# Kernel tuning notes

Hardware: AMD Instinct MI355X
Metric: run time of the kernel (lower is better)

The kernel has to match this reference:

```python
import jax, jax.numpy as jnp
import numpy as np

TRIANGLE_TABLE = np.array([
    [-1,-1,-1,-1,-1,-1],[1,0,2,-1,-1,-1],[4,0,3,-1,-1,-1],[1,4,2,1,3,4],
    [3,1,5,-1,-1,-1],[2,3,0,2,5,3],[1,4,0,1,5,4],[4,2,5,-1,-1,-1],
    [4,5,2,-1,-1,-1],[4,1,0,4,5,1],[3,2,0,3,5,2],[1,3,5,-1,-1,-1],
    [4,1,2,4,3,1],[3,0,4,-1,-1,-1],[2,0,1,-1,-1,-1],[-1,-1,-1,-1,-1,-1]], dtype=np.int32)
NUM_TRI_TABLE = np.array([0,1,1,2,1,2,2,1,1,2,2,1,2,1,1,0], dtype=np.int32)
BASE_TET_EDGES = np.array([0,1,0,2,0,3,1,2,1,3,2,3], dtype=np.int32)

NV = 200_000
NT = 800_000

def setup_inputs() -> dict:
    key = jax.random.key(0)
    k1, k2, k3 = jax.random.split(key, 3)
    pos_nx3 = jax.random.normal(k1, (NV, 3), dtype=jnp.float32)
    sdf_n = jax.random.normal(k2, (NV,), dtype=jnp.float32)
    tet_fx4 = jax.random.randint(k3, (NT, 4), 0, NV, dtype=jnp.int32)
    return {"pos_nx3": pos_nx3, "sdf_n": sdf_n, "tet_fx4": tet_fx4}

def map_uv(face_gidx, max_idx):
    # Faithful port of DMTet.map_uv: one 2-triangle UV quad per (potential) tet.
    N = int(np.ceil(np.sqrt((max_idx + 1) // 2)))
    lin = jnp.linspace(0.0, 1.0 - 1.0 / N, N, dtype=jnp.float32)
    tex_y, tex_x = jnp.meshgrid(lin, lin, indexing='ij')
    pad = 0.9 / N
    uvs = jnp.stack([tex_x, tex_y, tex_x + pad, tex_y,
                     tex_x + pad, tex_y + pad, tex_x, tex_y + pad], axis=-1).reshape(-1, 2)
    t = face_gidx // 2
    tet_idx = (t // N) * N + (t % N)   # identity for t < N*N, kept faithful
    tri_idx = face_gidx % 2
    uv_idx = jnp.stack([tet_idx * 4, tet_idx * 4 + tri_idx + 1, tet_idx * 4 + tri_idx + 2], axis=-1)
    return uvs, uv_idx.reshape(-1, 3)

def reference(pos_nx3, sdf_n, tet_fx4):
    # NOTE: marching-tets output sizes are data dependent -> eager (non-jit) jax,
    # matching the torch.unique / boolean-mask structure of the original.
    tri_table = jnp.asarray(TRIANGLE_TABLE)
    num_tri_table = jnp.asarray(NUM_TRI_TABLE)
    base_edges = jnp.asarray(BASE_TET_EDGES)

    occ_n = sdf_n > 0                                   # [Nv]
    occ_fx4 = occ_n[tet_fx4]                            # [T,4]
    occ_sum = occ_fx4.sum(-1)
    valid_tets = (occ_sum > 0) & (occ_sum < 4)

    tet_valid = tet_fx4[valid_tets]                     # [Tv,4]
    all_edges = tet_valid[:, base_edges].reshape(-1, 2) # [Tv*6,2]
    all_edges = jnp.sort(all_edges, axis=1)             # == sort_edges
    unique_edges, idx_map = jnp.unique(all_edges, axis=0, return_inverse=True)

    mask_edges = occ_n[unique_edges].sum(-1) == 1       # sign-crossing edges
    mapping = jnp.where(mask_edges, jnp.cumsum(mask_edges) - 1, -1)
    idx_map = mapping[idx_map.reshape(-1)].reshape(-1, 6)
    interp_v = unique_edges[mask_edges]                 # [Ne,2]

    # linear interpolation of crossing point along each edge
    p = pos_nx3[interp_v]                               # [Ne,2,3]
    s = sdf_n[interp_v] * jnp.array([1.0, -1.0], dtype=sdf_n.dtype)  # negate 2nd sdf
    denom = s.sum(1, keepdims=True)                     # [Ne,1]
    w = s[:, ::-1] / denom                              # flip + normalize
    verts = (p * w[:, :, None]).sum(1)                  # [Ne,3]

    v_id = jnp.array([1, 2, 4, 8], dtype=jnp.int32)
    tetindex = (occ_fx4[valid_tets].astype(jnp.int32) * v_id).sum(-1)  # [Tv]
    num_triangles = num_tri_table[tetindex]
    m1 = num_triangles == 1
    m2 = num_triangles == 2
    f1 = jnp.take_along_axis(idx_map[m1], tri_table[tetindex[m1]][:, :3], axis=1).reshape(-1, 3)
    f2 = jnp.take_along_axis(idx_map[m2], tri_table[tetindex[m2]][:, :6], axis=1).reshape(-1, 3)
    faces = jnp.concatenate([f1, f2], axis=0)

    num_tets = tet_fx4.shape[0]
    tet_gidx = jnp.arange(num_tets, dtype=jnp.int32)[valid_tets]
    face_gidx = jnp.concatenate([
        tet_gidx[m1] * 2,
        jnp.stack([tet_gidx[m2] * 2, tet_gidx[m2] * 2 + 1], axis=-1).reshape(-1)], axis=0)

    uvs, uv_idx = map_uv(face_gidx, num_tets * 2)
    return verts, faces, uvs, uv_idx
```

## Files before the change

### kernel.cpp

```cpp
#include <hip/hip_runtime.h>
#include <cstdio>
#include <cstdint>

typedef unsigned long long u64;

static const int kNV = 200000;
static const int kNT = 800000;
static const int kNUV = 895;
#define UVS_ROWS   3204100LL
#define UVS_FLOATS 6408200LL
#define CAP 3300000

#define NH 392
#define TILE_T 2048
#define BINW 64
#define BSH 6
#define NBIN 3125
#define SUBSH 15
#define FINEB 512
#define MAXBIN 2816
#define C 11

__device__ const int c_tri[16][6] = {
    {-1,-1,-1,-1,-1,-1},{1,0,2,-1,-1,-1},{4,0,3,-1,-1,-1},{1,4,2,1,3,4},
    {3,1,5,-1,-1,-1},{2,3,0,2,5,3},{1,4,0,1,5,4},{4,2,5,-1,-1,-1},
    {4,5,2,-1,-1,-1},{4,1,0,4,5,1},{3,2,0,3,5,2},{1,3,5,-1,-1,-1},
    {4,1,2,4,3,1},{3,0,4,-1,-1,-1},{2,0,1,-1,-1,-1},{-1,-1,-1,-1,-1,-1}};
__device__ const int c_ntri[16]   = {0,1,1,2,1,2,2,1,1,2,2,1,2,1,1,0};
__device__ const int c_ncross[16] = {0,3,3,4,3,4,4,3,3,4,4,3,4,3,3,0};
__device__ const int c_edges[12] = {0,1,0,2,0,3,1,2,1,3,2,3};

#define PK(m1,m2,nc) (((u64)(m1) << 44) | ((u64)(m2) << 24) | (u64)(nc))

__device__ __forceinline__ int blockScanExcl(int v, volatile int* wsum, int tid, int* totalOut){
  int lane = tid & 63, wv = tid >> 6;
  int x = v;
  #pragma unroll
  for (int off = 1; off < 64; off <<= 1){
    int t = __shfl_up(x, off, 64);
    if (lane >= off) x += t;
  }
  __syncthreads();
  if (lane == 63) wsum[wv] = x;
  __syncthreads();
  int carry = 0;
  #pragma unroll
  for (int w = 0; w < 4; w++) if (w < wv) carry += wsum[w];
  if (totalOut) *totalOut = wsum[0] + wsum[1] + wsum[2] + wsum[3];
  return carry + x - v;
}

#define SCAN_B 256
#define SCAN_I 8
#define SCAN_TILE (SCAN_B*SCAN_I)

template<typename T>
__global__ void k_scan_partial(const T* __restrict__ in, T* __restrict__ partials, int n){
  __shared__ T sm[SCAN_B];
  int b = blockIdx.x;
  long long base = (long long)b*SCAN_TILE;
  T sum = 0;
  for (int i = threadIdx.x; i < SCAN_TILE; i += SCAN_B){
    long long idx = base + i;
    if (idx < n) sum += in[idx];
  }
  sm[threadIdx.x] = sum; __syncthreads();
  for (int s = SCAN_B/2; s > 0; s >>= 1){
    if ((int)threadIdx.x < s) sm[threadIdx.x] += sm[threadIdx.x + s];
    __syncthreads();
  }
  if (threadIdx.x == 0) partials[b] = sm[0];
}

template<typename T>
__global__ void k_scan_blocksums(T* __restrict__ partials, int nb, T* __restrict__ total_out){
  __shared__ T sm[SCAN_B];
  T carry = 0;
  for (int base = 0; base < nb; base += SCAN_B){
    int i = base + (int)threadIdx.x;
    T v = (i < nb) ? partials[i] : (T)0;
    sm[threadIdx.x] = v; __syncthreads();
    for (int off = 1; off < SCAN_B; off <<= 1){
      T t = ((int)threadIdx.x >= off) ? sm[threadIdx.x - off] : (T)0;
      __syncthreads();
      sm[threadIdx.x] += t;
      __syncthreads();
    }
    if (i < nb) partials[i] = carry + sm[threadIdx.x] - v;
    T tilesum = sm[SCAN_B-1];
    __syncthreads();
    carry += tilesum;
  }
  if (threadIdx.x == 0 && total_out) *total_out = carry;
}

template<typename T>
__global__ void k_scan_apply(const T* __restrict__ in, T* __restrict__ out,
                             const T* __restrict__ partials, int n){
  __shared__ T sm[SCAN_B];
  int b = blockIdx.x;
  long long base = (long long)b*SCAN_TILE + (long long)threadIdx.x*SCAN_I;
  T v[SCAN_I]; T s = 0;
  #pragma unroll
  for (int k = 0; k < SCAN_I; k++){ long long idx = base + k; v[k] = (idx < n) ? in[idx] : (T)0; s += v[k]; }
  sm[threadIdx.x] = s; __syncthreads();
  for (int off = 1; off < 256; off <<= 1){
    T t = ((int)threadIdx.x >= off) ? sm[threadIdx.x - off] : (T)0;
    __syncthreads();
    sm[threadIdx.x] += t;
    __syncthreads();
  }
  T excl = sm[threadIdx.x] - s + partials[b];
  #pragma unroll
  for (int k = 0; k < SCAN_I; k++){ long long idx = base + k; if (idx < n) out[idx] = excl; excl += v[k]; }
}

template<typename T>
static void run_scan(const T* in, T* out, int n, T* partials, hipStream_t s){
  int nb = (n + SCAN_TILE - 1) / SCAN_TILE;
  k_scan_partial<T><<<nb, SCAN_B, 0, s>>>(in, partials, n);
  k_scan_blocksums<T><<<1, SCAN_B, 0, s>>>(partials, nb, out + n);
  k_scan_apply<T><<<nb, SCAN_B, 0, s>>>(in, out, partials, n);
}


__global__ void k_classify_hist(const int* __restrict__ tet, const float* __restrict__ sdf,
                                int* __restrict__ tetinfo, u64* __restrict__ pk,
                                int* __restrict__ blockHist, u64* __restrict__ pkPart){
  __shared__ int h[NBIN];
  __shared__ u64 red[256];
  int blk = blockIdx.x;
  for (int j = threadIdx.x; j < NBIN; j += 256) h[j] = 0;
  __syncthreads();
  int t0 = blk*TILE_T;
  u64 myPk = 0;
  for (int k = 0; k < TILE_T/256; k++){
    int t = t0 + k*256 + threadIdx.x;
    if (t < kNT){
      int4 v4 = ((const int4*)tet)[t];
      int pat = ((sdf[v4.x] > 0.0f) ? 1 : 0) | ((sdf[v4.y] > 0.0f) ? 2 : 0)
              | ((sdf[v4.z] > 0.0f) ? 4 : 0) | ((sdf[v4.w] > 0.0f) ? 8 : 0);
      tetinfo[t] = pat;
      int nt_ = c_ntri[pat];
      u64 pv = PK(nt_ == 1, nt_ == 2, c_ncross[pat]);
      pk[t] = pv;
      myPk += pv;
      if (pat != 0 && pat != 15){
        int vv[4] = {v4.x, v4.y, v4.z, v4.w};
        #pragma unroll
        for (int e = 0; e < 6; e++){
          int i0 = c_edges[2*e], i1 = c_edges[2*e+1];
          if (((pat >> i0) & 1) != ((pat >> i1) & 1)){
            int a = vv[i0], b = vv[i1]; if (a > b){ int tm = a; a = b; b = tm; }
            atomicAdd(&h[a >> BSH], 1);
          }
        }
      }
    }
  }
  red[threadIdx.x] = myPk;
  __syncthreads();
  for (int s = 128; s > 0; s >>= 1){
    if ((int)threadIdx.x < s) red[threadIdx.x] += red[threadIdx.x + s];
    __syncthreads();
  }
  if (threadIdx.x == 0) pkPart[blk] = red[0];
  for (int j = threadIdx.x; j < NBIN; j += 256) blockHist[j*NH + blk] = h[j];
}

__global__ void k_scatter(const int* __restrict__ tet, const int* __restrict__ tetinfo,
                          const u64* __restrict__ psum, const int* __restrict__ bhScan,
                          u64* __restrict__ ebin){
  __shared__ int c[NBIN];
  int blk = blockIdx.x;
  for (int j = threadIdx.x; j < NBIN; j += 256) c[j] = bhScan[j*NH + blk];
  __syncthreads();
  int t0 = blk*TILE_T;
  for (int k = 0; k < TILE_T/256; k++){
    int t = t0 + k*256 + threadIdx.x;
    if (t < kNT){
      int pat = tetinfo[t];
      if (pat != 0 && pat != 15){
        int4 v4 = ((const int4*)tet)[t];
        int vv[4] = {v4.x, v4.y, v4.z, v4.w};
        int seq = (int)(psum[t] & 0xFFFFFF);
        #pragma unroll
        for (int e = 0; e < 6; e++){
          int i0 = c_edges[2*e], i1 = c_edges[2*e+1];
          if (((pat >> i0) & 1) != ((pat >> i1) & 1)){
            int a = vv[i0], b = vv[i1]; if (a > b){ int tm = a; a = b; b = tm; }
            int pos = atomicAdd(&c[a >> BSH], 1);
            ebin[pos] = ((u64)(unsigned)a << 40) | ((u64)(unsigned)b << 22) | (unsigned)seq;
            seq++;
          }
        }
      }
    }
  }
}

__global__ void k_fineflags(const int* __restrict__ bhScan, const u64* __restrict__ ebin,
                            u64* __restrict__ efin, unsigned* __restrict__ meta,
                            int* __restrict__ binFirstCnt){
  __shared__ u64 ld[MAXBIN];
  __shared__ unsigned char fl[MAXBIN];
  __shared__ unsigned short fp[MAXBIN];
  __shared__ int h[FINEB];
  __shared__ int wsum[4];
  int bin = blockIdx.x, tid = threadIdx.x;
  int binStart = bhScan[bin*NH];
  int binEnd   = bhScan[(bin+1)*NH];
  int n = binEnd - binStart;
  int a0 = bin << BSH;
  for (int j = tid; j < FINEB; j += 256) h[j] = 0;
  __syncthreads();
  if (n <= MAXBIN){
    u64 pr[C]; int kr[C];
    #pragma unroll
    for (int k = 0; k < C; k++){
      int i = tid + k*256;
      if (i < n){
        u64 p = ebin[binStart + i];
        pr[k] = p;
        kr[k] = (((int)(p >> 40) - a0) << 3) | ((int)((p >> 22) & 0x3FFFF) >> SUBSH);
      } else kr[k] = -1;
    }
    #pragma unroll
    for (int k = 0; k < C; k++) if (kr[k] >= 0) atomicAdd(&h[kr[k]], 1);
    __syncthreads();
    int s0 = h[2*tid], s1 = h[2*tid+1];
    int excl = blockScanExcl(s0 + s1, wsum, tid, nullptr);
    h[2*tid] = excl; h[2*tid+1] = excl + s0;
    __syncthreads();
    #pragma unroll
    for (int k = 0; k < C; k++)
      if (kr[k] >= 0) ld[atomicAdd(&h[kr[k]], 1)] = pr[k];
    __syncthreads();
    #pragma unroll
    for (int k = 0; k < C; k++){
      int x = tid + k*256;
      if (x < n){
        u64 my = ld[x] >> 22;
        int key = (((int)(my >> 18) - a0) << 3) | ((int)(my & 0x3FFFF) >> SUBSH);
        int gs = key ? h[key-1] : 0;
        unsigned char f = 1;
        for (int y = x-1; y >= gs; y--){ if ((ld[y] >> 22) == my){ f = 0; break; } }
        fl[x] = f;
      } else if (x < MAXBIN) fl[x] = 0;
    }
    __syncthreads();
    int cbase = tid*C;
    int loc[C]; int cs = 0;
    #pragma unroll
    for (int q = 0; q < C; q++){ loc[q] = fl[cbase+q]; cs += loc[q]; }
    int tot;
    int ex2 = blockScanExcl(cs, wsum, tid, &tot);
    #pragma unroll
    for (int q = 0; q < C; q++){ fp[cbase+q] = (unsigned short)ex2; ex2 += loc[q]; }
    if (tid == 0) binFirstCnt[bin] = tot;
    __syncthreads();
    #pragma unroll
    for (int k = 0; k < C; k++){
      int x = tid + k*256;
      if (x < n){
        u64 p = ld[x];
        u64 my = p >> 22;
        int key = (((int)(my >> 18) - a0) << 3) | ((int)(my & 0x3FFFF) >> SUBSH);
        int gs = key ? h[key-1] : 0;
        int ge = h[key];
        int rk = 0;
        for (int y = gs; y < ge; y++){ if (fl[y] && (ld[y] >> 22) < my) rk++; }
        int rp = (int)fp[gs] + rk;
        efin[binStart + x] = p;
        meta[binStart + x] = ((unsigned)bin << 13) | ((unsigned)rp << 1) | (unsigned)fl[x];
      }
    }
  } else {
    for (int i = binStart + tid; i < binEnd; i += 256){
      u64 p = ebin[i];
      int key = (((int)(p >> 40) - a0) << 3) | ((int)((p >> 22) & 0x3FFFF) >> SUBSH);
      atomicAdd(&h[key], 1);
    }
    __syncthreads();
    int s0 = h[2*tid], s1 = h[2*tid+1];
    int excl = blockScanExcl(s0 + s1, wsum, tid, nullptr);
    h[2*tid] = excl; h[2*tid+1] = excl + s0;
    __syncthreads();
    for (int i = binStart + tid; i < binEnd; i += 256){
      u64 p = ebin[i];
      int key = (((int)(p >> 40) - a0) << 3) | ((int)((p >> 22) & 0x3FFFF) >> SUBSH);
      efin[binStart + atomicAdd(&h[key], 1)] = p;
    }
    __syncthreads();
    if (tid == 0){
      int fcnt = 0;
      for (int x = 0; x < n; x++){
        u64 key = efin[binStart+x] >> 22; u64 grp = key >> SUBSH;
        int sx = x; while (sx > 0 && ((efin[binStart+sx-1] >> 22) >> SUBSH) == grp) sx--;
        int f = 1;
        for (int y = sx; y < x; y++) if ((efin[binStart+y] >> 22) == key){ f = 0; break; }
        int fb = 0;
        for (int y = 0; y < sx; y++){
          u64 ky = efin[binStart+y] >> 22; u64 gy = ky >> SUBSH;
          int sy = y; while (sy > 0 && ((efin[binStart+sy-1] >> 22) >> SUBSH) == gy) sy--;
          int fy = 1;
          for (int z = sy; z < y; z++) if ((efin[binStart+z] >> 22) == ky){ fy = 0; break; }
          fb += fy;
        }
        int ex = x+1; while (ex < n && ((efin[binStart+ex] >> 22) >> SUBSH) == grp) ex++;
        int rk = 0;
        for (int y = sx; y < ex; y++){
          u64 ky = efin[binStart+y] >> 22;
          if (ky < key){
            int fy = 1;
            for (int z = sx; z < y; z++) if ((efin[binStart+z] >> 22) == ky){ fy = 0; break; }
            if (fy) rk++;
          }
        }
        if (f) fcnt++;
        meta[binStart+x] = ((unsigned)bin << 13) | ((unsigned)(fb+rk) << 1) | (unsigned)f;
      }
      binFirstCnt[bin] = fcnt;
    }
  }
}

__global__ void k_emit(const u64* __restrict__ efin, const int* __restrict__ totp,
                       const int* __restrict__ binPref, const unsigned* __restrict__ meta,
                       const float* __restrict__ pos, const float* __restrict__ sdf,
                       float* __restrict__ out, int* __restrict__ rankBySeq){
  int total = *totp;
  int i = blockIdx.x*256 + threadIdx.x;
  if (i >= total) return;
  u64 p = efin[i];
  unsigned m = meta[i];
  int first = m & 1;
  int rp = (m >> 1) & 0xFFF;
  int bin = m >> 13;
  int r = binPref[bin] + rp;
  rankBySeq[(int)(p & 0x3FFFFF)] = r;
  if (first){
    int a = (int)(p >> 40);
    int b = (int)((p >> 22) & 0x3FFFF);
    float sa = sdf[a], sb = sdf[b];
    float denom = sa - sb;
    float w0 = (-sb) / denom;
    float w1 = sa / denom;
    out[3LL*r + 0] = pos[3*a+0]*w0 + pos[3*b+0]*w1;
    out[3LL*r + 1] = pos[3*a+1]*w0 + pos[3*b+1]*w1;
    out[3LL*r + 2] = pos[3*a+2]*w0 + pos[3*b+2]*w1;
  }
}

__global__ void k_faces(const int* __restrict__ tetinfo, const u64* __restrict__ psum,
                        const int* __restrict__ Nep, const int* __restrict__ rankBySeq,
                        float* __restrict__ out){
  int t = blockIdx.x*256 + threadIdx.x; if (t >= kNT) return;
  int pat = tetinfo[t];
  int nt_ = c_ntri[pat];
  if (nt_ == 0) return;
  u64 tot = psum[kNT];
  int Nm1 = (int)(tot >> 44), Nm2 = (int)((tot >> 24) & 0xFFFFF);
  int Ne = *Nep;
  long long faces_off = 3LL*Ne;
  long long uvidx_off = faces_off + 3LL*((long long)Nm1 + 2LL*Nm2) + UVS_FLOATS;
  u64 ps = psum[t];
  int m1v = (int)(ps >> 44), m2v = (int)((ps >> 24) & 0xFFFFF);
  int seq = (int)(ps & 0xFFFFFF);
  int er[6];
  int j = 0;
  #pragma unroll
  for (int e = 0; e < 6; e++){
    int i0 = c_edges[2*e], i1 = c_edges[2*e+1];
    if (((pat >> i0) & 1) != ((pat >> i1) & 1)){
      er[e] = rankBySeq[seq + j];
      j++;
    } else er[e] = -1;
  }
  for (int k = 0; k < nt_; k++){
    long long row = (nt_ == 1) ? (long long)m1v : ((long long)Nm1 + 2LL*m2v + k);
    #pragma unroll
    for (int c = 0; c < 3; c++){
      int slot = c_tri[pat][3*k + c];
      out[faces_off + 3*row + c] = (float)er[slot];
    }
    out[uvidx_off + 3*row + 0] = (float)(4*t);
    out[uvidx_off + 3*row + 1] = (float)(4*t + k + 1);
    out[uvidx_off + 3*row + 2] = (float)(4*t + k + 2);
  }
}

__global__ void k_uvs(const u64* __restrict__ psum, const int* __restrict__ Nep,
                      float* __restrict__ out){
  long long r = (long long)blockIdx.x*256 + threadIdx.x;
  if (r >= UVS_ROWS) return;
  u64 tot = psum[kNT];
  int Nm1 = (int)(tot >> 44), Nm2 = (int)((tot >> 24) & 0xFFFFF);
  int Ne = *Nep;
  long long off = 3LL*Ne + 3LL*((long long)Nm1 + 2LL*Nm2);
  int cell = (int)(r >> 2), k = (int)(r & 3);
  int iy = cell / kNUV, ix = cell - iy*kNUV;
  const float delta = (1.0f - 1.0f/895.0f) / 894.0f;
  const float pad = 0.9f / 895.0f;
  float x = (float)ix * delta, y = (float)iy * delta;
  float u = x + ((k == 1 || k == 2) ? pad : 0.0f);
  float v = y + ((k >= 2) ? pad : 0.0f);
  if ((off & 1) == 0){
    float2 uv = make_float2(u, v);
    *reinterpret_cast<float2*>(&out[off + 2*r]) = uv;
  } else {
    out[off + 2*r]     = u;
    out[off + 2*r + 1] = v;
  }
}

static inline int divup(int a, int b){ return (a + b - 1) / b; }

extern "C" void kernel_launch(void* const* d_in, const int* in_sizes, int n_in,
                              void* d_out, int out_size, void* d_ws, size_t ws_size,
                              hipStream_t stream){
  const float* pos = (const float*)d_in[0];
  const float* sdf = (const float*)d_in[1];
  const int*   tet = (const int*)d_in[2];
  float* out = (float*)d_out;

  char* ws = (char*)d_ws;
  size_t off = 0;
  auto alloc = [&](size_t bytes) -> char* {
    char* p = ws + off; off += (bytes + 255) & ~(size_t)255; return p;
  };
  int* tetinfo     = (int*)alloc((size_t)kNT*4);
  u64* pk          = (u64*)alloc((size_t)kNT*8);
  u64* psum        = (u64*)alloc((size_t)(kNT+1)*8);
  int* blockHist   = (int*)alloc((size_t)NBIN*NH*4);
  int* bhScan      = (int*)alloc((size_t)(NBIN*NH+1)*4);
  u64* ebin        = (u64*)alloc((size_t)CAP*8);
  u64* efin        = (u64*)alloc((size_t)CAP*8);
  unsigned* meta   = (unsigned*)alloc((size_t)CAP*4);
  int* rankBySeq   = (int*)alloc((size_t)CAP*4);
  int* binFirstCnt = (int*)alloc((size_t)(NBIN+1)*4);
  u64* pkPart      = (u64*)alloc((size_t)NH*8);
  int* partI       = (int*)alloc(4096*4);
  if (off > ws_size){
    fprintf(stderr, "[dmtet] workspace too small: need %zu have %zu\n", off, ws_size);
    return;
  }

  k_classify_hist<<<NH, 256, 0, stream>>>(tet, sdf, tetinfo, pk, blockHist, pkPart);
  k_scan_blocksums<u64><<<1, SCAN_B, 0, stream>>>(pkPart, NH, psum + kNT);
  k_scan_apply<u64><<<divup(kNT,SCAN_TILE), SCAN_B, 0, stream>>>(pk, psum, pkPart, kNT);
  run_scan<int>(blockHist, bhScan, NBIN*NH, partI, stream);
  k_scatter<<<NH, 256, 0, stream>>>(tet, tetinfo, psum, bhScan, ebin);
  k_fineflags<<<NBIN, 256, 0, stream>>>(bhScan, ebin, efin, meta, binFirstCnt);
  k_scan_blocksums<int><<<1, SCAN_B, 0, stream>>>(binFirstCnt, NBIN, binFirstCnt + NBIN);
  k_emit<<<divup(CAP,256), 256, 0, stream>>>(efin, bhScan + NBIN*NH, binFirstCnt, meta,
                                             pos, sdf, out, rankBySeq);
  k_faces<<<divup(kNT,256), 256, 0, stream>>>(tetinfo, psum, binFirstCnt + NBIN, rankBySeq, out);
  k_uvs<<<divup((int)UVS_ROWS,256), 256, 0, stream>>>(psum, binFirstCnt + NBIN, out);
}
```

Measured before the change: 211.1 us.

## Write per-seq edge metadata directly and emit verts only for unique edges

The fine-flags kernel now writes a compact (bin, rank) word indexed by edge sequence number and stores only first-occurrence edges into a compacted per-bin array, instead of writing the full sorted edge list and meta arrays. The old emit kernel, which swept all edges to build rankBySeq, is replaced by a per-bin vertex kernel that touches only unique edges. The faces kernel resolves ranks through binPref plus the meta word. This removes a full-size efin write/read and a rankBySeq pass, at the cost of an extra binPref lookup per face edge and a simpler but quadratic serial fallback for oversized bins.

```diff
diff --git a/kernel.cpp b/kernel.cpp
--- a/kernel.cpp
+++ b/kernel.cpp
@@ -200,7 +200,7 @@
 }
 
 __global__ void k_fineflags(const int* __restrict__ bhScan, const u64* __restrict__ ebin,
-                            u64* __restrict__ efin, unsigned* __restrict__ meta,
+                            unsigned* __restrict__ metaBySeq, u64* __restrict__ vfirst,
                             int* __restrict__ binFirstCnt){
   __shared__ u64 ld[MAXBIN];
   __shared__ unsigned char fl[MAXBIN];
@@ -271,89 +271,59 @@
         int rk = 0;
         for (int y = gs; y < ge; y++){ if (fl[y] && (ld[y] >> 22) < my) rk++; }
         int rp = (int)fp[gs] + rk;
-        efin[binStart + x] = p;
-        meta[binStart + x] = ((unsigned)bin << 13) | ((unsigned)rp << 1) | (unsigned)fl[x];
+        metaBySeq[(int)(p & 0x3FFFFF)] = ((unsigned)bin << 12) | (unsigned)rp;
+        if (fl[x]) vfirst[binStart + rp] = p;
       }
     }
   } else {
-    for (int i = binStart + tid; i < binEnd; i += 256){
-      u64 p = ebin[i];
-      int key = (((int)(p >> 40) - a0) << 3) | ((int)((p >> 22) & 0x3FFFF) >> SUBSH);
-      atomicAdd(&h[key], 1);
-    }
-    __syncthreads();
-    int s0 = h[2*tid], s1 = h[2*tid+1];
-    int excl = blockScanExcl(s0 + s1, wsum, tid, nullptr);
-    h[2*tid] = excl; h[2*tid+1] = excl + s0;
-    __syncthreads();
-    for (int i = binStart + tid; i < binEnd; i += 256){
-      u64 p = ebin[i];
-      int key = (((int)(p >> 40) - a0) << 3) | ((int)((p >> 22) & 0x3FFFF) >> SUBSH);
-      efin[binStart + atomicAdd(&h[key], 1)] = p;
-    }
-    __syncthreads();
     if (tid == 0){
       int fcnt = 0;
       for (int x = 0; x < n; x++){
-        u64 key = efin[binStart+x] >> 22; u64 grp = key >> SUBSH;
-        int sx = x; while (sx > 0 && ((efin[binStart+sx-1] >> 22) >> SUBSH) == grp) sx--;
+        u64 px = ebin[binStart+x];
+        u64 kx = px >> 22;
         int f = 1;
-        for (int y = sx; y < x; y++) if ((efin[binStart+y] >> 22) == key){ f = 0; break; }
-        int fb = 0;
-        for (int y = 0; y < sx; y++){
-          u64 ky = efin[binStart+y] >> 22; u64 gy = ky >> SUBSH;
-          int sy = y; while (sy > 0 && ((efin[binStart+sy-1] >> 22) >> SUBSH) == gy) sy--;
-          int fy = 1;
-          for (int z = sy; z < y; z++) if ((efin[binStart+z] >> 22) == ky){ fy = 0; break; }
-          fb += fy;
-        }
-        int ex = x+1; while (ex < n && ((efin[binStart+ex] >> 22) >> SUBSH) == grp) ex++;
-        int rk = 0;
-        for (int y = sx; y < ex; y++){
-          u64 ky = efin[binStart+y] >> 22;
-          if (ky < key){
+        for (int y = 0; y < x; y++) if ((ebin[binStart+y] >> 22) == kx){ f = 0; break; }
+        int rp = 0;
+        for (int y = 0; y < n; y++){
+          u64 ky = ebin[binStart+y] >> 22;
+          if (ky < kx){
             int fy = 1;
-            for (int z = sx; z < y; z++) if ((efin[binStart+z] >> 22) == ky){ fy = 0; break; }
-            if (fy) rk++;
+            for (int z = 0; z < y; z++) if ((ebin[binStart+z] >> 22) == ky){ fy = 0; break; }
+            rp += fy;
           }
         }
-        if (f) fcnt++;
-        meta[binStart+x] = ((unsigned)bin << 13) | ((unsigned)(fb+rk) << 1) | (unsigned)f;
+        if (f){ vfirst[binStart + rp] = px; fcnt++; }
+        metaBySeq[(int)(px & 0x3FFFFF)] = ((unsigned)bin << 12) | (unsigned)rp;
       }
       binFirstCnt[bin] = fcnt;
     }
   }
 }
 
-__global__ void k_emit(const u64* __restrict__ efin, const int* __restrict__ totp,
-                       const int* __restrict__ binPref, const unsigned* __restrict__ meta,
-                       const float* __restrict__ pos, const float* __restrict__ sdf,
-                       float* __restrict__ out, int* __restrict__ rankBySeq){
-  int total = *totp;
-  int i = blockIdx.x*256 + threadIdx.x;
-  if (i >= total) return;
-  u64 p = efin[i];
-  unsigned m = meta[i];
-  int first = m & 1;
-  int rp = (m >> 1) & 0xFFF;
-  int bin = m >> 13;
-  int r = binPref[bin] + rp;
-  rankBySeq[(int)(p & 0x3FFFFF)] = r;
-  if (first){
+__global__ void k_verts(const int* __restrict__ bhScan, const u64* __restrict__ vfirst,
+                        const int* __restrict__ binPref, const float* __restrict__ pos,
+                        const float* __restrict__ sdf, float* __restrict__ out){
+  int bin = blockIdx.x;
+  int binStart = bhScan[bin*NH];
+  int rbase = binPref[bin];
+  int cnt = binPref[bin+1] - rbase;
+  for (int f = threadIdx.x; f < cnt; f += 256){
+    u64 p = vfirst[binStart + f];
     int a = (int)(p >> 40);
     int b = (int)((p >> 22) & 0x3FFFF);
     float sa = sdf[a], sb = sdf[b];
     float denom = sa - sb;
     float w0 = (-sb) / denom;
     float w1 = sa / denom;
-    out[3LL*r + 0] = pos[3*a+0]*w0 + pos[3*b+0]*w1;
-    out[3LL*r + 1] = pos[3*a+1]*w0 + pos[3*b+1]*w1;
-    out[3LL*r + 2] = pos[3*a+2]*w0 + pos[3*b+2]*w1;
+    long long r = rbase + f;
+    out[3*r + 0] = pos[3*a+0]*w0 + pos[3*b+0]*w1;
+    out[3*r + 1] = pos[3*a+1]*w0 + pos[3*b+1]*w1;
+    out[3*r + 2] = pos[3*a+2]*w0 + pos[3*b+2]*w1;
   }
 }
 
 __global__ void k_faces(const int* __restrict__ tetinfo, const u64* __restrict__ psum,
-                        const int* __restrict__ Nep, const int* __restrict__ rankBySeq,
+                        const int* __restrict__ binPref, const unsigned* __restrict__ metaBySeq,
                         float* __restrict__ out){
   int t = blockIdx.x*256 + threadIdx.x; if (t >= kNT) return;
   int pat = tetinfo[t];
@@ -361,7 +331,7 @@
   if (nt_ == 0) return;
   u64 tot = psum[kNT];
   int Nm1 = (int)(tot >> 44), Nm2 = (int)((tot >> 24) & 0xFFFFF);
-  int Ne = *Nep;
+  int Ne = binPref[NBIN];
   long long faces_off = 3LL*Ne;
   long long uvidx_off = faces_off + 3LL*((long long)Nm1 + 2LL*Nm2) + UVS_FLOATS;
   u64 ps = psum[t];
@@ -373,7 +343,8 @@
   for (int e = 0; e < 6; e++){
     int i0 = c_edges[2*e], i1 = c_edges[2*e+1];
     if (((pat >> i0) & 1) != ((pat >> i1) & 1)){
-      er[e] = rankBySeq[seq + j];
+      unsigned m = metaBySeq[seq + j];
+      er[e] = binPref[m >> 12] + (int)(m & 0xFFF);
       j++;
     } else er[e] = -1;
   }
@@ -390,13 +361,13 @@
   }
 }
 
-__global__ void k_uvs(const u64* __restrict__ psum, const int* __restrict__ Nep,
+__global__ void k_uvs(const u64* __restrict__ psum, const int* __restrict__ binPref,
                       float* __restrict__ out){
   long long r = (long long)blockIdx.x*256 + threadIdx.x;
   if (r >= UVS_ROWS) return;
   u64 tot = psum[kNT];
   int Nm1 = (int)(tot >> 44), Nm2 = (int)((tot >> 24) & 0xFFFFF);
-  int Ne = *Nep;
+  int Ne = binPref[NBIN];
   long long off = 3LL*Ne + 3LL*((long long)Nm1 + 2LL*Nm2);
   int cell = (int)(r >> 2), k = (int)(r & 3);
   int iy = cell / kNUV, ix = cell - iy*kNUV;
@@ -429,18 +400,17 @@
   auto alloc = [&](size_t bytes) -> char* {
     char* p = ws + off; off += (bytes + 255) & ~(size_t)255; return p;
   };
-  int* tetinfo     = (int*)alloc((size_t)kNT*4);
-  u64* pk          = (u64*)alloc((size_t)kNT*8);
-  u64* psum        = (u64*)alloc((size_t)(kNT+1)*8);
-  int* blockHist   = (int*)alloc((size_t)NBIN*NH*4);
-  int* bhScan      = (int*)alloc((size_t)(NBIN*NH+1)*4);
-  u64* ebin        = (u64*)alloc((size_t)CAP*8);
-  u64* efin        = (u64*)alloc((size_t)CAP*8);
-  unsigned* meta   = (unsigned*)alloc((size_t)CAP*4);
-  int* rankBySeq   = (int*)alloc((size_t)CAP*4);
-  int* binFirstCnt = (int*)alloc((size_t)(NBIN+1)*4);
-  u64* pkPart      = (u64*)alloc((size_t)NH*8);
-  int* partI       = (int*)alloc(4096*4);
+  int* tetinfo      = (int*)alloc((size_t)kNT*4);
+  u64* pk           = (u64*)alloc((size_t)kNT*8);
+  u64* psum         = (u64*)alloc((size_t)(kNT+1)*8);
+  int* blockHist    = (int*)alloc((size_t)NBIN*NH*4);
+  int* bhScan       = (int*)alloc((size_t)(NBIN*NH+1)*4);
+  u64* ebin         = (u64*)alloc((size_t)CAP*8);
+  u64* vfirst       = (u64*)alloc((size_t)CAP*8);
+  unsigned* metaBySeq = (unsigned*)alloc((size_t)CAP*4);
+  int* binFirstCnt  = (int*)alloc((size_t)(NBIN+1)*4);
+  u64* pkPart       = (u64*)alloc((size_t)NH*8);
+  int* partI        = (int*)alloc(4096*4);
   if (off > ws_size){
     fprintf(stderr, "[dmtet] workspace too small: need %zu have %zu\n", off, ws_size);
     return;
@@ -451,10 +421,9 @@
   k_scan_apply<u64><<<divup(kNT,SCAN_TILE), SCAN_B, 0, stream>>>(pk, psum, pkPart, kNT);
   run_scan<int>(blockHist, bhScan, NBIN*NH, partI, stream);
   k_scatter<<<NH, 256, 0, stream>>>(tet, tetinfo, psum, bhScan, ebin);
-  k_fineflags<<<NBIN, 256, 0, stream>>>(bhScan, ebin, efin, meta, binFirstCnt);
+  k_fineflags<<<NBIN, 256, 0, stream>>>(bhScan, ebin, metaBySeq, vfirst, binFirstCnt);
   k_scan_blocksums<int><<<1, SCAN_B, 0, stream>>>(binFirstCnt, NBIN, binFirstCnt + NBIN);
-  k_emit<<<divup(CAP,256), 256, 0, stream>>>(efin, bhScan + NBIN*NH, binFirstCnt, meta,
-                                             pos, sdf, out, rankBySeq);
-  k_faces<<<divup(kNT,256), 256, 0, stream>>>(tetinfo, psum, binFirstCnt + NBIN, rankBySeq, out);
-  k_uvs<<<divup((int)UVS_ROWS,256), 256, 0, stream>>>(psum, binFirstCnt + NBIN, out);
-}
+  k_verts<<<NBIN, 256, 0, stream>>>(bhScan, vfirst, binFirstCnt, pos, sdf, out);
+  k_faces<<<divup(kNT,256), 256, 0, stream>>>(tetinfo, psum, binFirstCnt, metaBySeq, out);
+  k_uvs<<<divup((int)UVS_ROWS,256), 256, 0, stream>>>(psum, binFirstCnt, out);
+}
```

Result: faster. 204.9 us (-2.9%).
